# Optimization experiments

Hardware: AMD Instinct MI355X
Metric: run time of the kernel (lower is better)

The kernel has to match this reference:

```python
import jax, jax.numpy as jnp
import numpy as np

DIM = 512
H = 8
D = DIM // H  # head_dim = 64
B, N = 2, 2048


def setup_inputs() -> dict:
    key = jax.random.key(0)
    ks = jax.random.split(key, 12)
    s = 1.0 / np.sqrt(DIM)
    inp = {
        "x": jax.random.normal(ks[0], (B, N, DIM), jnp.float32),
        "geo_bias": jax.random.normal(ks[1], (B, H, N, N), jnp.float32),
        "Wq": jax.random.normal(ks[2], (DIM, DIM), jnp.float32) * s,
        "bq": jnp.zeros((DIM,), jnp.float32),
        "Wk": jax.random.normal(ks[3], (DIM, DIM), jnp.float32) * s,
        "bk": jnp.zeros((DIM,), jnp.float32),
        "Wv": jax.random.normal(ks[4], (DIM, DIM), jnp.float32) * s,
        "bv": jnp.zeros((DIM,), jnp.float32),
        "Wo": jax.random.normal(ks[5], (DIM, DIM), jnp.float32) * s,
        "bo": jnp.zeros((DIM,), jnp.float32),
    }
    return inp


def reference(x, geo_bias, Wq, bq, Wk, bk, Wv, bv, Wo, bo):
    # x: (B, N, dim); geo_bias: (B, H, N, N)
    scale = D ** -0.5
    q = (x @ Wq.T + bq).reshape(B, N, H, D)
    k = (x @ Wk.T + bk).reshape(B, N, H, D)
    v = (x @ Wv.T + bv).reshape(B, N, H, D)
    # scores: (B, H, N, N)
    attn = jnp.einsum("bihd,bjhd->bhij", q, k) * scale + geo_bias
    attn = jax.nn.softmax(attn, axis=-1)
    out = jnp.einsum("bhij,bjhd->bihd", attn, v).reshape(B, N, DIM)
    return out @ Wo.T + bo
```

## Files before the change

kernel.cpp:

```cpp
#include <hip/hip_runtime.h>
#include <math.h>

#define Bb 2
#define Nn 2048
#define DIMM 512
#define Hh 8
#define DHd 64
#define SCALE 0.125f

typedef __bf16 bf16;
typedef __bf16 bf16x8 __attribute__((ext_vector_type(8)));
typedef float f32x4 __attribute__((ext_vector_type(4)));

#define WS_XB   0u
#define WS_WB   4194304u
#define WS_Q    6291456u
#define WS_K    10485760u
#define WS_VT   14680064u
#define WS_AT   18874368u

__global__ __launch_bounds__(256) void convert_kernel(
    const float* __restrict__ x, const float* __restrict__ wq,
    const float* __restrict__ wk, const float* __restrict__ wv,
    const float* __restrict__ wo, bf16* __restrict__ xb, bf16* __restrict__ wb) {
  int i = blockIdx.x * 256 + threadIdx.x;
  const float4* src; bf16* dst; int off;
  if (i < 524288) { src = (const float4*)x; dst = xb; off = i; }
  else {
    int j = i - 524288;
    int wsel = j >> 16; off = j & 65535;
    const float* wl = wsel == 0 ? wq : wsel == 1 ? wk : wsel == 2 ? wv : wo;
    src = (const float4*)wl; dst = wb + (wsel << 18);
  }
  float4 v = src[off];
  union { bf16 h[4]; uint2 u; } tmp;
  tmp.h[0] = (bf16)v.x; tmp.h[1] = (bf16)v.y;
  tmp.h[2] = (bf16)v.z; tmp.h[3] = (bf16)v.w;
  ((uint2*)dst)[off] = tmp.u;
}

__global__ __launch_bounds__(256) void qkv_gemm(
    const bf16* __restrict__ xb, const bf16* __restrict__ wb,
    const float* __restrict__ bq, const float* __restrict__ bk,
    const float* __restrict__ bv, bf16* __restrict__ qws,
    bf16* __restrict__ kws, bf16* __restrict__ vtws) {
  __shared__ bf16 Al[128 * 40];
  __shared__ bf16 Bl[128 * 40];
  int t = threadIdx.x;
  int m0 = (blockIdx.x & 31) << 7;
  int n0 = (blockIdx.x >> 5) << 7;
  int lane = t & 63, w = t >> 6;
  int quad = lane >> 4, col = lane & 15;
  int mblk = (w >> 1) * 64, nblk = (w & 1) * 64;
  f32x4 acc[4][4] = {};
  for (int k0 = 0; k0 < 512; k0 += 32) {
    __syncthreads();
    for (int pass = 0; pass < 2; ++pass) {
      int c = t + (pass << 8);
      int row = c >> 2, part = c & 3;
      *(uint4*)&Al[row * 40 + part * 8] =
          *(const uint4*)&xb[(m0 + row) * 512 + k0 + part * 8];
      *(uint4*)&Bl[row * 40 + part * 8] =
          *(const uint4*)&wb[(n0 + row) * 512 + k0 + part * 8];
    }
    __syncthreads();
    bf16x8 af[4], bfv[4];
    for (int i = 0; i < 4; i++)
      af[i] = *(const bf16x8*)&Al[(mblk + i * 16 + col) * 40 + quad * 8];
    for (int i = 0; i < 4; i++)
      bfv[i] = *(const bf16x8*)&Bl[(nblk + i * 16 + col) * 40 + quad * 8];
    for (int mi = 0; mi < 4; mi++)
      for (int ni = 0; ni < 4; ni++)
        acc[mi][ni] = __builtin_amdgcn_mfma_f32_16x16x32_bf16(
            af[mi], bfv[ni], acc[mi][ni], 0, 0, 0);
  }
  for (int mi = 0; mi < 4; mi++)
    for (int ni = 0; ni < 4; ni++)
      for (int r = 0; r < 4; r++) {
        int m = m0 + mblk + mi * 16 + quad * 4 + r;
        int n = n0 + nblk + ni * 16 + col;
        int wid = n >> 9, feat = n & 511;
        float bias = wid == 0 ? bq[feat] : wid == 1 ? bk[feat] : bv[feat];
        bf16 v = (bf16)(acc[mi][ni][r] + bias);
        int bidx = m >> 11, seq = m & 2047;
        int h = feat >> 6, d = feat & 63;
        if (wid == 2)
          vtws[((((bidx << 3) + h) << 6) + d) * 2048 + seq] = v;
        else {
          bf16* dst = wid == 0 ? qws : kws;
          dst[((((bidx << 3) + h) << 11) + seq) * 64 + d] = v;
        }
      }
}

__global__ __launch_bounds__(256) void attn_kernel(
    const bf16* __restrict__ qws, const bf16* __restrict__ kws,
    const bf16* __restrict__ vtws, const float* __restrict__ gbias,
    bf16* __restrict__ attn) {
  __shared__ bf16 Kl[64 * 72];
  __shared__ bf16 Vl[64 * 72];
  __shared__ bf16 Pl[64 * 72];
  int t = threadIdx.x, lane = t & 63, w = t >> 6;
  int quad = lane >> 4, col = lane & 15;
  int bh = blockIdx.x >> 5, qt = blockIdx.x & 31;
  int q0 = qt << 6;
  const bf16* qbase = qws + (size_t)bh * 2048 * 64;
  const bf16* kbase = kws + (size_t)bh * 2048 * 64;
  const bf16* vbase = vtws + (size_t)bh * 64 * 2048;
  const float* bb = gbias + ((size_t)bh * 2048 + q0) * 2048;

  bf16x8 aq[2];
  for (int ks = 0; ks < 2; ++ks)
    aq[ks] = *(const bf16x8*)&qbase[(q0 + w * 16 + col) * 64 + ks * 32 + quad * 8];

  f32x4 o[4] = {};
  float mrow[4], lrow[4];
  for (int r = 0; r < 4; r++) { mrow[r] = -INFINITY; lrow[r] = 0.f; }

  for (int kt = 0; kt < 32; ++kt) {
    int s0 = kt << 6;
    __syncthreads();
    for (int pass = 0; pass < 2; ++pass) {
      int c = t + (pass << 8);
      int row = c >> 3, part = c & 7;
      *(uint4*)&Kl[row * 72 + part * 8] =
          *(const uint4*)&kbase[(s0 + row) * 64 + part * 8];
      *(uint4*)&Vl[row * 72 + part * 8] =
          *(const uint4*)&vbase[row * 2048 + s0 + part * 8];
    }
    __syncthreads();
    f32x4 s[4];
    for (int nt = 0; nt < 4; ++nt) {
      f32x4 a = {};
      for (int ks = 0; ks < 2; ++ks) {
        bf16x8 bk_ = *(const bf16x8*)&Kl[(nt * 16 + col) * 72 + ks * 32 + quad * 8];
        a = __builtin_amdgcn_mfma_f32_16x16x32_bf16(aq[ks], bk_, a, 0, 0, 0);
      }
      s[nt] = a;
    }
    float p[4][4];
    for (int r = 0; r < 4; r++) {
      int gq = w * 16 + quad * 4 + r;
      const float* brow = bb + (size_t)gq * 2048 + s0;
      float sv[4];
      float mx = -INFINITY;
      for (int nt = 0; nt < 4; nt++) {
        sv[nt] = s[nt][r] * SCALE + brow[nt * 16 + col];
        mx = fmaxf(mx, sv[nt]);
      }
      for (int d = 1; d < 16; d <<= 1) mx = fmaxf(mx, __shfl_xor(mx, d));
      float mnew = fmaxf(mrow[r], mx);
      float alpha = __expf(mrow[r] - mnew);
      float sum = 0.f;
      for (int nt = 0; nt < 4; nt++) {
        float e = __expf(sv[nt] - mnew);
        p[nt][r] = e; sum += e;
      }
      for (int d = 1; d < 16; d <<= 1) sum += __shfl_xor(sum, d);
      lrow[r] = lrow[r] * alpha + sum;
      mrow[r] = mnew;
      for (int dt = 0; dt < 4; ++dt) o[dt][r] *= alpha;
    }
    for (int nt = 0; nt < 4; nt++)
      for (int r = 0; r < 4; r++)
        Pl[(w * 16 + quad * 4 + r) * 72 + nt * 16 + col] = (bf16)p[nt][r];
    __syncthreads();
    for (int ks = 0; ks < 2; ++ks) {
      bf16x8 ap = *(const bf16x8*)&Pl[(w * 16 + col) * 72 + ks * 32 + quad * 8];
      for (int dt = 0; dt < 4; ++dt) {
        bf16x8 bv_ = *(const bf16x8*)&Vl[(dt * 16 + col) * 72 + ks * 32 + quad * 8];
        o[dt] = __builtin_amdgcn_mfma_f32_16x16x32_bf16(ap, bv_, o[dt], 0, 0, 0);
      }
    }
  }
  bf16* obase = attn + (size_t)(bh >> 3) * 2048 * 512 + (bh & 7) * 64;
  for (int r = 0; r < 4; r++) {
    float inv = 1.f / lrow[r];
    int gq = q0 + w * 16 + quad * 4 + r;
    for (int dt = 0; dt < 4; ++dt)
      obase[(size_t)gq * 512 + dt * 16 + col] = (bf16)(o[dt][r] * inv);
  }
}

__global__ __launch_bounds__(256) void out_gemm(
    const bf16* __restrict__ ab, const bf16* __restrict__ wob,
    const float* __restrict__ bo, float* __restrict__ out) {
  __shared__ bf16 Al[128 * 40];
  __shared__ bf16 Bl[128 * 40];
  int t = threadIdx.x;
  int m0 = (blockIdx.x & 31) << 7;
  int n0 = (blockIdx.x >> 5) << 7;
  int lane = t & 63, w = t >> 6;
  int quad = lane >> 4, col = lane & 15;
  int mblk = (w >> 1) * 64, nblk = (w & 1) * 64;
  f32x4 acc[4][4] = {};
  for (int k0 = 0; k0 < 512; k0 += 32) {
    __syncthreads();
    for (int pass = 0; pass < 2; ++pass) {
      int c = t + (pass << 8);
      int row = c >> 2, part = c & 3;
      *(uint4*)&Al[row * 40 + part * 8] =
          *(const uint4*)&ab[(m0 + row) * 512 + k0 + part * 8];
      *(uint4*)&Bl[row * 40 + part * 8] =
          *(const uint4*)&wob[(n0 + row) * 512 + k0 + part * 8];
    }
    __syncthreads();
    bf16x8 af[4], bfv[4];
    for (int i = 0; i < 4; i++)
      af[i] = *(const bf16x8*)&Al[(mblk + i * 16 + col) * 40 + quad * 8];
    for (int i = 0; i < 4; i++)
      bfv[i] = *(const bf16x8*)&Bl[(nblk + i * 16 + col) * 40 + quad * 8];
    for (int mi = 0; mi < 4; mi++)
      for (int ni = 0; ni < 4; ni++)
        acc[mi][ni] = __builtin_amdgcn_mfma_f32_16x16x32_bf16(
            af[mi], bfv[ni], acc[mi][ni], 0, 0, 0);
  }
  for (int mi = 0; mi < 4; mi++)
    for (int ni = 0; ni < 4; ni++)
      for (int r = 0; r < 4; r++) {
        int m = m0 + mblk + mi * 16 + quad * 4 + r;
        int n = n0 + nblk + ni * 16 + col;
        out[(size_t)m * 512 + n] = acc[mi][ni][r] + bo[n];
      }
}

extern "C" void kernel_launch(void* const* d_in, const int* in_sizes, int n_in,
                              void* d_out, int out_size, void* d_ws, size_t ws_size,
                              hipStream_t stream) {
  const float* x  = (const float*)d_in[0];
  const float* gb = (const float*)d_in[1];
  const float* Wq = (const float*)d_in[2];
  const float* bq = (const float*)d_in[3];
  const float* Wk = (const float*)d_in[4];
  const float* bk = (const float*)d_in[5];
  const float* Wv = (const float*)d_in[6];
  const float* bv = (const float*)d_in[7];
  const float* Wo = (const float*)d_in[8];
  const float* bo = (const float*)d_in[9];
  float* out = (float*)d_out;
  char* ws = (char*)d_ws;
  bf16* xb   = (bf16*)(ws + WS_XB);
  bf16* wb   = (bf16*)(ws + WS_WB);
  bf16* qws  = (bf16*)(ws + WS_Q);
  bf16* kws  = (bf16*)(ws + WS_K);
  bf16* vtws = (bf16*)(ws + WS_VT);
  bf16* at   = (bf16*)(ws + WS_AT);

  hipLaunchKernelGGL(convert_kernel, dim3(3072), dim3(256), 0, stream,
                     x, Wq, Wk, Wv, Wo, xb, wb);
  hipLaunchKernelGGL(qkv_gemm, dim3(384), dim3(256), 0, stream,
                     xb, wb, bq, bk, bv, qws, kws, vtws);
  hipLaunchKernelGGL(attn_kernel, dim3(512), dim3(256), 0, stream,
                     qws, kws, vtws, gb, at);
  hipLaunchKernelGGL(out_gemm, dim3(128), dim3(256), 0, stream,
                     at, wb + 3 * 262144, bo, out);
}
```

Baseline: 444.9 us.

## Double-buffer K/V tiles and prefetch geo bias in attention kernel

The attention kernel now double-buffers K and V in shared memory. The next tile's global loads are issued into registers before the current tile's MFMAs, and a barrier is removed per iteration. Geo-bias values are prefetched two tiles ahead into registers, so the biggest memory stream overlaps with compute. The QKV epilogue packs four V-transpose values into one 8-byte store, and launch bounds now ask for two blocks per CU. Costs are more registers and LDS, plus a harmless over-read past the last tile.

```diff
diff --git a/kernel.cpp b/kernel.cpp
--- a/kernel.cpp
+++ b/kernel.cpp
@@ -1,11 +1,6 @@
 #include <hip/hip_runtime.h>
 #include <math.h>
 
-#define Bb 2
-#define Nn 2048
-#define DIMM 512
-#define Hh 8
-#define DHd 64
 #define SCALE 0.125f
 
 typedef __bf16 bf16;
@@ -75,30 +70,32 @@
             af[mi], bfv[ni], acc[mi][ni], 0, 0, 0);
   }
   for (int mi = 0; mi < 4; mi++)
-    for (int ni = 0; ni < 4; ni++)
-      for (int r = 0; r < 4; r++) {
-        int m = m0 + mblk + mi * 16 + quad * 4 + r;
-        int n = n0 + nblk + ni * 16 + col;
-        int wid = n >> 9, feat = n & 511;
-        float bias = wid == 0 ? bq[feat] : wid == 1 ? bk[feat] : bv[feat];
-        bf16 v = (bf16)(acc[mi][ni][r] + bias);
-        int bidx = m >> 11, seq = m & 2047;
-        int h = feat >> 6, d = feat & 63;
-        if (wid == 2)
-          vtws[((((bidx << 3) + h) << 6) + d) * 2048 + seq] = v;
-        else {
-          bf16* dst = wid == 0 ? qws : kws;
-          dst[((((bidx << 3) + h) << 11) + seq) * 64 + d] = v;
-        }
-      }
-}
-
-__global__ __launch_bounds__(256) void attn_kernel(
+    for (int ni = 0; ni < 4; ni++) {
+      int n = n0 + nblk + ni * 16 + col;
+      int wid = n >> 9, feat = n & 511;
+      float bias = wid == 0 ? bq[feat] : wid == 1 ? bk[feat] : bv[feat];
+      int h = feat >> 6, d = feat & 63;
+      int mbase = m0 + mblk + mi * 16 + quad * 4;
+      int bidx = mbase >> 11, seq0 = mbase & 2047;
+      if (wid == 2) {
+        union { bf16 h4[4]; ushort4 u4; } pk;
+        for (int r = 0; r < 4; r++) pk.h4[r] = (bf16)(acc[mi][ni][r] + bias);
+        *(ushort4*)&vtws[(size_t)((((bidx << 3) + h) << 6) + d) * 2048 + seq0] = pk.u4;
+      } else {
+        bf16* dst = wid == 0 ? qws : kws;
+        for (int r = 0; r < 4; r++)
+          dst[(size_t)((((bidx << 3) + h) << 11) + seq0 + r) * 64 + d] =
+              (bf16)(acc[mi][ni][r] + bias);
+      }
+    }
+}
+
+__global__ __launch_bounds__(256, 2) void attn_kernel(
     const bf16* __restrict__ qws, const bf16* __restrict__ kws,
     const bf16* __restrict__ vtws, const float* __restrict__ gbias,
     bf16* __restrict__ attn) {
-  __shared__ bf16 Kl[64 * 72];
-  __shared__ bf16 Vl[64 * 72];
+  __shared__ bf16 Kl[2][64 * 72];
+  __shared__ bf16 Vl[2][64 * 72];
   __shared__ bf16 Pl[64 * 72];
   int t = threadIdx.x, lane = t & 63, w = t >> 6;
   int quad = lane >> 4, col = lane & 15;
@@ -109,6 +106,9 @@
   const bf16* vbase = vtws + (size_t)bh * 64 * 2048;
   const float* bb = gbias + ((size_t)bh * 2048 + q0) * 2048;
 
+  int srow = t >> 2;
+  int scol = (t & 3) << 4;
+
   bf16x8 aq[2];
   for (int ks = 0; ks < 2; ++ks)
     aq[ks] = *(const bf16x8*)&qbase[(q0 + w * 16 + col) * 64 + ks * 32 + quad * 8];
@@ -117,62 +117,110 @@
   float mrow[4], lrow[4];
   for (int r = 0; r < 4; r++) { mrow[r] = -INFINITY; lrow[r] = 0.f; }
 
-  for (int kt = 0; kt < 32; ++kt) {
-    int s0 = kt << 6;
-    __syncthreads();
-    for (int pass = 0; pass < 2; ++pass) {
-      int c = t + (pass << 8);
-      int row = c >> 3, part = c & 7;
-      *(uint4*)&Kl[row * 72 + part * 8] =
-          *(const uint4*)&kbase[(s0 + row) * 64 + part * 8];
-      *(uint4*)&Vl[row * 72 + part * 8] =
-          *(const uint4*)&vbase[row * 2048 + s0 + part * 8];
-    }
-    __syncthreads();
-    f32x4 s[4];
-    for (int nt = 0; nt < 4; ++nt) {
-      f32x4 a = {};
+  float bc[2][16];
+  for (int r = 0; r < 4; r++)
+    for (int nt = 0; nt < 4; nt++) {
+      const float* brow = bb + (size_t)(w * 16 + quad * 4 + r) * 2048;
+      bc[0][r * 4 + nt] = brow[nt * 16 + col];
+      bc[1][r * 4 + nt] = brow[64 + nt * 16 + col];
+    }
+
+  {
+    *(uint4*)&Kl[0][srow * 72 + scol]     = *(const uint4*)&kbase[srow * 64 + scol];
+    *(uint4*)&Kl[0][srow * 72 + scol + 8] = *(const uint4*)&kbase[srow * 64 + scol + 8];
+    *(uint4*)&Vl[0][srow * 72 + scol]     = *(const uint4*)&vbase[srow * 2048 + scol];
+    *(uint4*)&Vl[0][srow * 72 + scol + 8] = *(const uint4*)&vbase[srow * 2048 + scol + 8];
+  }
+  __syncthreads();
+
+  for (int kt = 0; kt < 32; kt += 2) {
+#pragma unroll
+    for (int u = 0; u < 2; ++u) {
+      const int cur = u;
+      int kt_ = kt + u;
+      int snxt = (kt_ + 1) << 6;
+
+      uint4 kra = *(const uint4*)&kbase[(snxt + srow) * 64 + scol];
+      uint4 krb = *(const uint4*)&kbase[(snxt + srow) * 64 + scol + 8];
+      uint4 vra = *(const uint4*)&vbase[srow * 2048 + snxt + scol];
+      uint4 vrb = *(const uint4*)&vbase[srow * 2048 + snxt + scol + 8];
+
+      f32x4 s[4];
+#pragma unroll
+      for (int nt = 0; nt < 4; ++nt) {
+        f32x4 a = {};
+#pragma unroll
+        for (int ks = 0; ks < 2; ++ks) {
+          bf16x8 bk_ = *(const bf16x8*)&Kl[cur][(nt * 16 + col) * 72 + ks * 32 + quad * 8];
+          a = __builtin_amdgcn_mfma_f32_16x16x32_bf16(aq[ks], bk_, a, 0, 0, 0);
+        }
+        s[nt] = a;
+      }
+
+      float p[4][4];
+#pragma unroll
+      for (int r = 0; r < 4; r++) {
+        float sv[4];
+        float mx = -INFINITY;
+#pragma unroll
+        for (int nt = 0; nt < 4; nt++) {
+          sv[nt] = s[nt][r] * SCALE + bc[cur][r * 4 + nt];
+          mx = fmaxf(mx, sv[nt]);
+        }
+#pragma unroll
+        for (int d = 1; d < 16; d <<= 1) mx = fmaxf(mx, __shfl_xor(mx, d));
+        float mnew = fmaxf(mrow[r], mx);
+        float alpha = __expf(mrow[r] - mnew);
+        float sum = 0.f;
+#pragma unroll
+        for (int nt = 0; nt < 4; nt++) {
+          float e = __expf(sv[nt] - mnew);
+          p[nt][r] = e; sum += e;
+        }
+#pragma unroll
+        for (int d = 1; d < 16; d <<= 1) sum += __shfl_xor(sum, d);
+        lrow[r] = lrow[r] * alpha + sum;
+        mrow[r] = mnew;
+#pragma unroll
+        for (int dt = 0; dt < 4; ++dt) o[dt][r] *= alpha;
+      }
+
+      if (kt_ < 30) {
+        int sb = (kt_ + 2) << 6;
+#pragma unroll
+        for (int r = 0; r < 4; r++) {
+          const float* brow = bb + (size_t)(w * 16 + quad * 4 + r) * 2048 + sb;
+#pragma unroll
+          for (int nt = 0; nt < 4; nt++)
+            bc[cur][r * 4 + nt] = brow[nt * 16 + col];
+        }
+      }
+
+#pragma unroll
+      for (int nt = 0; nt < 4; nt++)
+#pragma unroll
+        for (int r = 0; r < 4; r++)
+          Pl[(w * 16 + quad * 4 + r) * 72 + nt * 16 + col] = (bf16)p[nt][r];
+
+#pragma unroll
       for (int ks = 0; ks < 2; ++ks) {
-        bf16x8 bk_ = *(const bf16x8*)&Kl[(nt * 16 + col) * 72 + ks * 32 + quad * 8];
-        a = __builtin_amdgcn_mfma_f32_16x16x32_bf16(aq[ks], bk_, a, 0, 0, 0);
-      }
-      s[nt] = a;
-    }
-    float p[4][4];
-    for (int r = 0; r < 4; r++) {
-      int gq = w * 16 + quad * 4 + r;
-      const float* brow = bb + (size_t)gq * 2048 + s0;
-      float sv[4];
-      float mx = -INFINITY;
-      for (int nt = 0; nt < 4; nt++) {
-        sv[nt] = s[nt][r] * SCALE + brow[nt * 16 + col];
-        mx = fmaxf(mx, sv[nt]);
-      }
-      for (int d = 1; d < 16; d <<= 1) mx = fmaxf(mx, __shfl_xor(mx, d));
-      float mnew = fmaxf(mrow[r], mx);
-      float alpha = __expf(mrow[r] - mnew);
-      float sum = 0.f;
-      for (int nt = 0; nt < 4; nt++) {
-        float e = __expf(sv[nt] - mnew);
-        p[nt][r] = e; sum += e;
-      }
-      for (int d = 1; d < 16; d <<= 1) sum += __shfl_xor(sum, d);
-      lrow[r] = lrow[r] * alpha + sum;
-      mrow[r] = mnew;
-      for (int dt = 0; dt < 4; ++dt) o[dt][r] *= alpha;
-    }
-    for (int nt = 0; nt < 4; nt++)
-      for (int r = 0; r < 4; r++)
-        Pl[(w * 16 + quad * 4 + r) * 72 + nt * 16 + col] = (bf16)p[nt][r];
-    __syncthreads();
-    for (int ks = 0; ks < 2; ++ks) {
-      bf16x8 ap = *(const bf16x8*)&Pl[(w * 16 + col) * 72 + ks * 32 + quad * 8];
-      for (int dt = 0; dt < 4; ++dt) {
-        bf16x8 bv_ = *(const bf16x8*)&Vl[(dt * 16 + col) * 72 + ks * 32 + quad * 8];
-        o[dt] = __builtin_amdgcn_mfma_f32_16x16x32_bf16(ap, bv_, o[dt], 0, 0, 0);
-      }
-    }
-  }
+        bf16x8 ap = *(const bf16x8*)&Pl[(w * 16 + col) * 72 + ks * 32 + quad * 8];
+#pragma unroll
+        for (int dt = 0; dt < 4; ++dt) {
+          bf16x8 bv_ = *(const bf16x8*)&Vl[cur][(dt * 16 + col) * 72 + ks * 32 + quad * 8];
+          o[dt] = __builtin_amdgcn_mfma_f32_16x16x32_bf16(ap, bv_, o[dt], 0, 0, 0);
+        }
+      }
+
+      int nb = 1 - cur;
+      *(uint4*)&Kl[nb][srow * 72 + scol]     = kra;
+      *(uint4*)&Kl[nb][srow * 72 + scol + 8] = krb;
+      *(uint4*)&Vl[nb][srow * 72 + scol]     = vra;
+      *(uint4*)&Vl[nb][srow * 72 + scol + 8] = vrb;
+      __syncthreads();
+    }
+  }
+
   bf16* obase = attn + (size_t)(bh >> 3) * 2048 * 512 + (bh & 7) * 64;
   for (int r = 0; r < 4; r++) {
     float inv = 1.f / lrow[r];
```

After: 440.2 us. About the same (-1.1%).
